# Kernel tuning notes

Hardware: AMD Instinct MI355X
Metric: run time of the kernel (lower is better)

Reference implementation:

```python
import jax, jax.numpy as jnp
import numpy as np
from jax import lax

MAX_CHARS = 50
EMB_DIM = 16
VOCAB = 263 + 1  # +1 padding row as in the torch module
FILTERS = [(1, 32), (2, 32), (3, 64), (4, 128), (5, 256), (6, 512), (7, 1024)]
TOTAL_FILTERS = sum(nf for _, nf in FILTERS)  # 2048
HIDDEN = 768
B, S = 8, 512


def setup_inputs() -> dict:
    key = jax.random.key(0)
    ks = list(jax.random.split(key, 32))
    pop = lambda: ks.pop()
    inp = {}
    inp["input_ids"] = jax.random.randint(pop(), (B, S, MAX_CHARS), 0, VOCAB, dtype=jnp.int32)
    inp["char_emb"] = jax.random.normal(pop(), (VOCAB, EMB_DIM), dtype=jnp.float32) * 0.02
    for i, (w, nf) in enumerate(FILTERS):
        inp[f"conv_w{i}"] = jax.random.normal(pop(), (nf, EMB_DIM, w), dtype=jnp.float32) * 0.05
        inp[f"conv_b{i}"] = jax.random.normal(pop(), (nf,), dtype=jnp.float32) * 0.02
    for j in range(2):  # highway layers, gate-bias half initialized to 1 as in torch code
        inp[f"hw_w{j}"] = jax.random.normal(pop(), (TOTAL_FILTERS, 2 * TOTAL_FILTERS), dtype=jnp.float32) * 0.02
        b_nl = jax.random.normal(pop(), (TOTAL_FILTERS,), dtype=jnp.float32) * 0.02
        inp[f"hw_b{j}"] = jnp.concatenate([b_nl, jnp.ones((TOTAL_FILTERS,), jnp.float32)])
    inp["proj_w"] = jax.random.normal(pop(), (TOTAL_FILTERS, HIDDEN), dtype=jnp.float32) * 0.02
    inp["proj_b"] = jax.random.normal(pop(), (HIDDEN,), dtype=jnp.float32) * 0.02
    return inp


def _char_cnn(input_ids, char_emb, conv_ws, conv_bs, hw_ws, hw_bs, proj_w, proj_b):
    token_dims = input_ids.shape[:-1]
    ids = input_ids.reshape(-1, MAX_CHARS)                     # [N, 50]
    x = char_emb[ids]                                          # [N, 50, 16]
    x = jnp.transpose(x, (0, 2, 1))                            # [N, C=16, L=50]
    outs = []
    for w_k, b_k in zip(conv_ws, conv_bs):
        y = lax.conv_general_dilated(x, w_k, window_strides=(1,), padding='VALID',
                                     dimension_numbers=('NCH', 'OIH', 'NCH'))
        y = y + b_k[None, :, None]                             # [N, nf, L-w+1]
        y = jax.nn.relu(jnp.max(y, axis=-1))                   # max-pool over positions, then relu
        outs.append(y)
    t = jnp.concatenate(outs, axis=-1)                         # [N, 2048]
    for hw_w, hw_b in zip(hw_ws, hw_bs):
        p = t @ hw_w + hw_b
        nl, gate = jnp.split(p, 2, axis=-1)
        g = jax.nn.sigmoid(gate)
        t = g * t + (1.0 - g) * jax.nn.relu(nl)
    out = t @ proj_w + proj_b                                  # [N, 768]
    return out.reshape(*token_dims, HIDDEN)


def reference(input_ids, char_emb,
              conv_w0, conv_b0, conv_w1, conv_b1, conv_w2, conv_b2, conv_w3, conv_b3,
              conv_w4, conv_b4, conv_w5, conv_b5, conv_w6, conv_b6,
              hw_w0, hw_b0, hw_w1, hw_b1, proj_w, proj_b):
    conv_ws = [conv_w0, conv_w1, conv_w2, conv_w3, conv_w4, conv_w5, conv_w6]
    conv_bs = [conv_b0, conv_b1, conv_b2, conv_b3, conv_b4, conv_b5, conv_b6]
    return _char_cnn(input_ids, char_emb, conv_ws, conv_bs,
                     [hw_w0, hw_w1], [hw_b0, hw_b1], proj_w, proj_b)
```

## Files before the change

kernel.cpp:

```cpp
#include <hip/hip_runtime.h>
#include <math.h>


#define NTOK 4096
#define NCHAR 50
#define EMB 16
#define TF 2048
#define HID 768
#define BK 64

typedef float f32x4 __attribute__((ext_vector_type(4)));
typedef _Float16 f16x8 __attribute__((ext_vector_type(8)));
typedef _Float16 half_t;

__device__ __forceinline__ void gl_lds16(const void* g, void* l) {
  __builtin_amdgcn_global_load_lds(
      (const __attribute__((address_space(1))) void*)g,
      (__attribute__((address_space(3))) void*)l, 16, 0, 0);
}

__global__ __launch_bounds__(256) void wpack_kernel(
    const float* __restrict__ w0, const float* __restrict__ w1,
    const float* __restrict__ w2, const float* __restrict__ w3,
    const float* __restrict__ w4, const float* __restrict__ w5,
    const float* __restrict__ w6,
    const float* __restrict__ b0, const float* __restrict__ b1,
    const float* __restrict__ b2, const float* __restrict__ b3,
    const float* __restrict__ b4, const float* __restrict__ b5,
    const float* __restrict__ b6,
    half_t* __restrict__ Wp, float* __restrict__ bias_all) {
  const int idx = blockIdx.x * 256 + threadIdx.x;
  if (idx < 219136) {
    int c, k, w; const float* src;
    if (idx < 1024)       { c = idx >> 5;             k = idx & 31;          w = 1; src = w0; }
    else if (idx < 2048)  { const int t = idx - 1024;  c = t >> 5; k = t & 31;  w = 2; src = w1; }
    else if (idx < 6144)  { const int t = idx - 2048;  c = t >> 6; k = t & 63;  w = 3; src = w2; }
    else if (idx < 14336) { const int t = idx - 6144;  c = t >> 6; k = t & 63;  w = 4; src = w3; }
    else if (idx < 38912) { const int t = idx - 14336; c = t / 96; k = t % 96;  w = 5; src = w4; }
    else if (idx < 88064) { const int t = idx - 38912; c = t / 96; k = t % 96;  w = 6; src = w5; }
    else                  { const int t = idx - 88064; c = t >> 7; k = t & 127; w = 7; src = w6; }
    const int j = k >> 4, i = k & 15;
    Wp[idx] = (half_t)((j < w) ? src[(c * EMB + i) * w + j] : 0.f);
  } else if (idx < 219136 + 2048) {
    const int c = idx - 219136;
    float v;
    if (c < 32)        v = b0[c];
    else if (c < 64)   v = b1[c - 32];
    else if (c < 128)  v = b2[c - 64];
    else if (c < 256)  v = b3[c - 128];
    else if (c < 512)  v = b4[c - 256];
    else if (c < 1024) v = b5[c - 512];
    else               v = b6[c - 1024];
    bias_all[c] = v;
  }
}


template<int MT, int KK, int NT, int L>
__device__ __forceinline__ void conv_mfma_worker(
    const char* myemb, float* pm,
    const half_t* __restrict__ Wp, const float* __restrict__ bias,
    half_t* __restrict__ outp, int kpad, int lane) {
  constexpr int S = NT * 16 + 8;
  const int l15 = lane & 15, l16 = lane >> 4;

  f16x8 a[MT][KK];
#pragma unroll
  for (int m = 0; m < MT; ++m)
#pragma unroll
    for (int kk = 0; kk < KK; ++kk) {
      const int row = m * 16 + l15 + 2 * kk + (l16 >> 1);
      a[m][kk] = *(const f16x8*)(myemb + row * 48 + (l16 & 1) * 16);
    }
#pragma unroll
  for (int m = 0; m < MT; ++m)
#pragma unroll
    for (int kk = 0; kk < KK; ++kk)
      asm volatile("" : "+v"(a[m][kk]));

  const half_t* bp = Wp + (size_t)l15 * kpad + l16 * 8;
  const size_t ntstep = (size_t)16 * kpad;

  auto group = [&](int nt, const f16x8 (&b)[KK]) {
    f32x4 acc[MT];
#pragma unroll
    for (int m = 0; m < MT; ++m) acc[m] = (f32x4){0.f, 0.f, 0.f, 0.f};
#pragma unroll
    for (int kk = 0; kk < KK; ++kk)
#pragma unroll
      for (int m = 0; m < MT; ++m)
        acc[m] = __builtin_amdgcn_mfma_f32_16x16x32_f16(a[m][kk], b[kk], acc[m], 0, 0, 0);
    float t[MT * 4];
#pragma unroll
    for (int m = 0; m < MT; ++m)
#pragma unroll
      for (int j = 0; j < 4; ++j) {
        const int pos = m * 16 + l16 * 4 + j;
        if ((m * 16 + 15) < L)
          t[m * 4 + j] = acc[m][j];
        else
          t[m * 4 + j] = (pos < L) ? acc[m][j] : -1e30f;
      }
#pragma unroll
    for (int s = 1; s < MT * 4; s *= 2)
#pragma unroll
      for (int i = 0; i + s < MT * 4; i += 2 * s)
        t[i] = fmaxf(t[i], t[i + s]);
    pm[l16 * S + nt * 16 + l15] = t[0];
  };

  f16x8 b0[KK], b1[KK];
#pragma unroll
  for (int kk = 0; kk < KK; ++kk) b0[kk] = *(const f16x8*)(bp + kk * 32);
#pragma unroll
  for (int nt = 0; nt < NT; nt += 2) {
#pragma unroll
    for (int kk = 0; kk < KK; ++kk)
      b1[kk] = *(const f16x8*)(bp + (size_t)(nt + 1) * ntstep + kk * 32);
    group(nt, b0);
    if (nt + 2 < NT) {
#pragma unroll
      for (int kk = 0; kk < KK; ++kk)
        b0[kk] = *(const f16x8*)(bp + (size_t)(nt + 2) * ntstep + kk * 32);
    }
    group(nt + 1, b1);
  }

#pragma unroll
  for (int c0 = 0; c0 < NT * 16; c0 += 64) {
    const int c = c0 + lane;
    if (c < NT * 16) {
      const float v0 = pm[0 * S + c], v1 = pm[1 * S + c];
      const float v2 = pm[2 * S + c], v3 = pm[3 * S + c];
      const float mx = fmaxf(fmaxf(v0, v1), fmaxf(v2, v3));
      outp[c] = (half_t)fmaxf(mx + bias[c], 0.f);
    }
  }
}

__global__ __launch_bounds__(256, 4) void conv_kernel(
    const int* __restrict__ ids, const float* __restrict__ cemb,
    const half_t* __restrict__ Wp, const float* __restrict__ bias_all,
    half_t* __restrict__ tout) {
  __shared__ char emb_s[4 * 72 * 48];
  __shared__ float pmax_s[4 * 4 * 264];
  const int tid = threadIdx.x, wave = tid >> 6, lane = tid & 63;
  const int tok = blockIdx.x * 4 + wave;
  char* myemb = emb_s + wave * (72 * 48);
  float* pm = pmax_s + wave * (4 * 264);

  for (int r = lane; r < 72; r += 64) {
    f16x8 lo, hi;
#pragma unroll
    for (int q = 0; q < 8; ++q) { lo[q] = (half_t)0.f; hi[q] = (half_t)0.f; }
    if (r < NCHAR) {
      const int id = ids[tok * NCHAR + r];
      const float4 v0 = *(const float4*)&cemb[id * EMB + 0];
      const float4 v1 = *(const float4*)&cemb[id * EMB + 4];
      const float4 v2 = *(const float4*)&cemb[id * EMB + 8];
      const float4 v3 = *(const float4*)&cemb[id * EMB + 12];
      lo[0] = (half_t)v0.x; lo[1] = (half_t)v0.y; lo[2] = (half_t)v0.z; lo[3] = (half_t)v0.w;
      lo[4] = (half_t)v1.x; lo[5] = (half_t)v1.y; lo[6] = (half_t)v1.z; lo[7] = (half_t)v1.w;
      hi[0] = (half_t)v2.x; hi[1] = (half_t)v2.y; hi[2] = (half_t)v2.z; hi[3] = (half_t)v2.w;
      hi[4] = (half_t)v3.x; hi[5] = (half_t)v3.y; hi[6] = (half_t)v3.z; hi[7] = (half_t)v3.w;
    }
    *(f16x8*)(myemb + r * 48) = lo;
    *(f16x8*)(myemb + r * 48 + 16) = hi;
  }

  half_t* outp = tout + (size_t)tok * TF;
  switch (blockIdx.y) {
    case 0:
      conv_mfma_worker<4, 1, 2, 50>(myemb, pm, Wp + 0,    bias_all + 0,   outp + 0,   32, lane);
      conv_mfma_worker<4, 1, 2, 49>(myemb, pm, Wp + 1024, bias_all + 32,  outp + 32,  32, lane);
      conv_mfma_worker<3, 2, 4, 48>(myemb, pm, Wp + 2048, bias_all + 64,  outp + 64,  64, lane);
      conv_mfma_worker<3, 2, 8, 47>(myemb, pm, Wp + 6144, bias_all + 128, outp + 128, 64, lane);
      break;
    case 1:  conv_mfma_worker<3, 3, 16, 46>(myemb, pm, Wp + 14336,  bias_all + 256,  outp + 256,  96,  lane); break;
    case 2:  conv_mfma_worker<3, 3, 16, 45>(myemb, pm, Wp + 38912,  bias_all + 512,  outp + 512,  96,  lane); break;
    case 3:  conv_mfma_worker<3, 3, 16, 45>(myemb, pm, Wp + 63488,  bias_all + 768,  outp + 768,  96,  lane); break;
    case 4:  conv_mfma_worker<3, 4, 16, 44>(myemb, pm, Wp + 88064,  bias_all + 1024, outp + 1024, 128, lane); break;
    case 5:  conv_mfma_worker<3, 4, 16, 44>(myemb, pm, Wp + 120832, bias_all + 1280, outp + 1280, 128, lane); break;
    case 6:  conv_mfma_worker<3, 4, 16, 44>(myemb, pm, Wp + 153600, bias_all + 1536, outp + 1536, 128, lane); break;
    default: conv_mfma_worker<3, 4, 16, 44>(myemb, pm, Wp + 186368, bias_all + 1792, outp + 1792, 128, lane); break;
  }
}

__global__ __launch_bounds__(256) void tcvt_kernel(
    const float* __restrict__ src, half_t* __restrict__ dst, int R, int C) {
  __shared__ half_t tile[64][72];
  const int tid = threadIdx.x;
  const int r0 = blockIdx.y * 64, c0 = blockIdx.x * 64;
  const int rr = tid >> 4, cq = tid & 15;
#pragma unroll
  for (int p = 0; p < 4; ++p) {
    const int r = rr + p * 16;
    const float4 v = *(const float4*)&src[(size_t)(r0 + r) * C + c0 + cq * 4];
    tile[cq * 4 + 0][r] = (half_t)v.x;
    tile[cq * 4 + 1][r] = (half_t)v.y;
    tile[cq * 4 + 2][r] = (half_t)v.z;
    tile[cq * 4 + 3][r] = (half_t)v.w;
  }
  __syncthreads();
#pragma unroll
  for (int p = 0; p < 2; ++p) {
    const int item = p * 256 + tid;
    const int c = item >> 3, ch = item & 7;
    const f16x8 v = *(const f16x8*)&tile[c][ch * 8];
    *(f16x8*)&dst[(size_t)(c0 + c) * R + r0 + ch * 8] = v;
  }
}

__global__ __launch_bounds__(256, 2) void highway_kernel(
    const half_t* __restrict__ tin, const half_t* __restrict__ Wt,
    const float* __restrict__ bv, half_t* __restrict__ tout) {
  __shared__ half_t smA[128 * BK];
  __shared__ half_t smBn[128 * BK];
  __shared__ half_t smBg[128 * BK];
  const int tid = threadIdx.x;
  const int wave = tid >> 6, lane = tid & 63;
  const int l15 = lane & 15, l16 = lane >> 4;
  const int wr = wave >> 1, wc = wave & 1;
  const int m0 = blockIdx.y * 128, n0 = blockIdx.x * 128;

  const char* Ab  = (const char*)tin + (size_t)m0 * (TF * 2);
  const char* Bnb = (const char*)Wt + (size_t)n0 * (TF * 2);
  const char* Bgb = (const char*)Wt + (size_t)(n0 + TF) * (TF * 2);

  f32x4 accn[4][4] = {};
  f32x4 accg[4][4] = {};

  for (int kt = 0; kt < TF / BK; ++kt) {
    if (kt) __syncthreads();
    const int kb0 = kt * (BK * 2);
#pragma unroll
    for (int i = 0; i < 4; ++i) {
      const int o = i * 4096 + tid * 16;
      const int row = o >> 7, kb = o & 127;
      const size_t gsrc = (size_t)row * (TF * 2) + kb0 + kb;
      gl_lds16(Ab + gsrc,  (char*)smA  + i * 4096 + wave * 1024);
      gl_lds16(Bnb + gsrc, (char*)smBn + i * 4096 + wave * 1024);
      gl_lds16(Bgb + gsrc, (char*)smBg + i * 4096 + wave * 1024);
    }
    __syncthreads();
#pragma unroll
    for (int ks = 0; ks < 2; ++ks) {
      f16x8 af[4], bn_[4], bg_[4];
#pragma unroll
      for (int m = 0; m < 4; ++m) {
        const int row = wr * 64 + m * 16 + l15;
        af[m] = *(const f16x8*)((const char*)smA + row * 128 + ks * 64 + l16 * 16);
      }
#pragma unroll
      for (int n = 0; n < 4; ++n) {
        const int row = wc * 64 + n * 16 + l15;
        bn_[n] = *(const f16x8*)((const char*)smBn + row * 128 + ks * 64 + l16 * 16);
        bg_[n] = *(const f16x8*)((const char*)smBg + row * 128 + ks * 64 + l16 * 16);
      }
#pragma unroll
      for (int m = 0; m < 4; ++m)
#pragma unroll
        for (int n = 0; n < 4; ++n) {
          accn[m][n] = __builtin_amdgcn_mfma_f32_16x16x32_f16(af[m], bn_[n], accn[m][n], 0, 0, 0);
          accg[m][n] = __builtin_amdgcn_mfma_f32_16x16x32_f16(af[m], bg_[n], accg[m][n], 0, 0, 0);
        }
    }
  }

#pragma unroll
  for (int n = 0; n < 4; ++n) {
    const int gn = n0 + wc * 64 + n * 16 + l15;
    const float bnl = bv[gn];
    const float bgt = bv[TF + gn];
#pragma unroll
    for (int m = 0; m < 4; ++m) {
#pragma unroll
      for (int j = 0; j < 4; ++j) {
        const int gm = m0 + wr * 64 + m * 16 + l16 * 4 + j;
        const float nl = accn[m][n][j] + bnl;
        const float gt = accg[m][n][j] + bgt;
        const float g = 1.f / (1.f + __expf(-gt));
        const float told = (float)tin[(size_t)gm * TF + gn];
        const float o = g * told + (1.f - g) * fmaxf(nl, 0.f);
        tout[(size_t)gm * TF + gn] = (half_t)o;
      }
    }
  }
}

__global__ __launch_bounds__(256, 2) void proj_kernel(
    const half_t* __restrict__ tin, const half_t* __restrict__ Wt,
    const float* __restrict__ bv, float* __restrict__ out) {
  __shared__ half_t smA[128 * BK];
  __shared__ half_t smB[128 * BK];
  const int tid = threadIdx.x;
  const int wave = tid >> 6, lane = tid & 63;
  const int l15 = lane & 15, l16 = lane >> 4;
  const int wr = wave >> 1, wc = wave & 1;
  const int m0 = blockIdx.y * 128, n0 = blockIdx.x * 128;

  const char* Ab = (const char*)tin + (size_t)m0 * (TF * 2);
  const char* Bb = (const char*)Wt + (size_t)n0 * (TF * 2);

  f32x4 acc[4][4] = {};

  for (int kt = 0; kt < TF / BK; ++kt) {
    if (kt) __syncthreads();
    const int kb0 = kt * (BK * 2);
#pragma unroll
    for (int i = 0; i < 4; ++i) {
      const int o = i * 4096 + tid * 16;
      const int row = o >> 7, kb = o & 127;
      const size_t gsrc = (size_t)row * (TF * 2) + kb0 + kb;
      gl_lds16(Ab + gsrc, (char*)smA + i * 4096 + wave * 1024);
      gl_lds16(Bb + gsrc, (char*)smB + i * 4096 + wave * 1024);
    }
    __syncthreads();
#pragma unroll
    for (int ks = 0; ks < 2; ++ks) {
      f16x8 af[4], bf[4];
#pragma unroll
      for (int m = 0; m < 4; ++m) {
        const int row = wr * 64 + m * 16 + l15;
        af[m] = *(const f16x8*)((const char*)smA + row * 128 + ks * 64 + l16 * 16);
      }
#pragma unroll
      for (int n = 0; n < 4; ++n) {
        const int row = wc * 64 + n * 16 + l15;
        bf[n] = *(const f16x8*)((const char*)smB + row * 128 + ks * 64 + l16 * 16);
      }
#pragma unroll
      for (int m = 0; m < 4; ++m)
#pragma unroll
        for (int n = 0; n < 4; ++n)
          acc[m][n] = __builtin_amdgcn_mfma_f32_16x16x32_f16(af[m], bf[n], acc[m][n], 0, 0, 0);
    }
  }

#pragma unroll
  for (int n = 0; n < 4; ++n) {
    const int gn = n0 + wc * 64 + n * 16 + l15;
    const float bb = bv[gn];
#pragma unroll
    for (int m = 0; m < 4; ++m) {
#pragma unroll
      for (int j = 0; j < 4; ++j) {
        const int gm = m0 + wr * 64 + m * 16 + l16 * 4 + j;
        out[(size_t)gm * HID + gn] = acc[m][n][j] + bb;
      }
    }
  }
}

extern "C" void kernel_launch(void* const* d_in, const int* in_sizes, int n_in,
                              void* d_out, int out_size, void* d_ws, size_t ws_size,
                              hipStream_t stream) {
  const int*   ids  = (const int*)d_in[0];
  const float* cemb = (const float*)d_in[1];
  const float* cw[7]; const float* cb[7];
  for (int i = 0; i < 7; ++i) {
    cw[i] = (const float*)d_in[2 + 2 * i];
    cb[i] = (const float*)d_in[3 + 2 * i];
  }
  const float* hw_w0  = (const float*)d_in[16];
  const float* hw_b0  = (const float*)d_in[17];
  const float* hw_w1  = (const float*)d_in[18];
  const float* hw_b1  = (const float*)d_in[19];
  const float* proj_w = (const float*)d_in[20];
  const float* proj_b = (const float*)d_in[21];
  float* out = (float*)d_out;

  char* ws = (char*)d_ws;
  half_t* t0h      = (half_t*)(ws);
  half_t* t1h      = (half_t*)(ws + 16777216);
  half_t* wbuf     = (half_t*)(ws + 33554432);
  float*  bias_all = (float*)(ws + 50331648);
  half_t* Wp       = (half_t*)(ws + 50339840);

  wpack_kernel<<<864, 256, 0, stream>>>(
      cw[0], cw[1], cw[2], cw[3], cw[4], cw[5], cw[6],
      cb[0], cb[1], cb[2], cb[3], cb[4], cb[5], cb[6], Wp, bias_all);

  conv_kernel<<<dim3(NTOK / 4, 8), 256, 0, stream>>>(ids, cemb, Wp, bias_all, t0h);

  tcvt_kernel<<<dim3(4096 / 64, TF / 64), 256, 0, stream>>>(hw_w0, wbuf, TF, 4096);
  highway_kernel<<<dim3(TF / 128, NTOK / 128), 256, 0, stream>>>(t0h, wbuf, hw_b0, t1h);

  tcvt_kernel<<<dim3(4096 / 64, TF / 64), 256, 0, stream>>>(hw_w1, wbuf, TF, 4096);
  highway_kernel<<<dim3(TF / 128, NTOK / 128), 256, 0, stream>>>(t1h, wbuf, hw_b1, t0h);

  tcvt_kernel<<<dim3(HID / 64, TF / 64), 256, 0, stream>>>(proj_w, wbuf, TF, HID);
  proj_kernel<<<dim3(HID / 128, NTOK / 128), 256, 0, stream>>>(t0h, wbuf, proj_b, out);
}
```

Measured before the change: 519.5 us.

## Pre-swizzle conv weights and GEMM LDS tiles into MFMA fragment order

Conv weights are packed so each lane's 16-byte B fragment for a given (nt, kk) sits contiguously, making the per-lane weight loads fully coalesced. The highway and projection GEMMs now fill LDS in 16x32 fragment blocks, so each wave reads its MFMA operands as linear 16-byte-per-lane chunks instead of row-strided 128-byte rows. The aim is to cut LDS bank conflicts and uncoalesced global reads. The packing index math grows, and the global loads feeding LDS become somewhat less contiguous per row.

```diff
diff --git a/kernel.cpp b/kernel.cpp
--- a/kernel.cpp
+++ b/kernel.cpp
@@ -19,7 +19,7 @@
       (__attribute__((address_space(3))) void*)l, 16, 0, 0);
 }
 
-__global__ __launch_bounds__(256) void wpack_kernel(
+__global__ __launch_bounds__(256) void wpack2_kernel(
     const float* __restrict__ w0, const float* __restrict__ w1,
     const float* __restrict__ w2, const float* __restrict__ w3,
     const float* __restrict__ w4, const float* __restrict__ w5,
@@ -28,19 +28,24 @@
     const float* __restrict__ b2, const float* __restrict__ b3,
     const float* __restrict__ b4, const float* __restrict__ b5,
     const float* __restrict__ b6,
-    half_t* __restrict__ Wp, float* __restrict__ bias_all) {
+    half_t* __restrict__ Wp2, float* __restrict__ bias_all) {
   const int idx = blockIdx.x * 256 + threadIdx.x;
   if (idx < 219136) {
-    int c, k, w; const float* src;
-    if (idx < 1024)       { c = idx >> 5;             k = idx & 31;          w = 1; src = w0; }
-    else if (idx < 2048)  { const int t = idx - 1024;  c = t >> 5; k = t & 31;  w = 2; src = w1; }
-    else if (idx < 6144)  { const int t = idx - 2048;  c = t >> 6; k = t & 63;  w = 3; src = w2; }
-    else if (idx < 14336) { const int t = idx - 6144;  c = t >> 6; k = t & 63;  w = 4; src = w3; }
-    else if (idx < 38912) { const int t = idx - 14336; c = t / 96; k = t % 96;  w = 5; src = w4; }
-    else if (idx < 88064) { const int t = idx - 38912; c = t / 96; k = t % 96;  w = 6; src = w5; }
-    else                  { const int t = idx - 88064; c = t >> 7; k = t & 127; w = 7; src = w6; }
+    int t, w, kpad; const float* src;
+    if (idx < 1024)       { t = idx;          w = 1; kpad = 32;  src = w0; }
+    else if (idx < 2048)  { t = idx - 1024;   w = 2; kpad = 32;  src = w1; }
+    else if (idx < 6144)  { t = idx - 2048;   w = 3; kpad = 64;  src = w2; }
+    else if (idx < 14336) { t = idx - 6144;   w = 4; kpad = 64;  src = w3; }
+    else if (idx < 38912) { t = idx - 14336;  w = 5; kpad = 96;  src = w4; }
+    else if (idx < 88064) { t = idx - 38912;  w = 6; kpad = 96;  src = w5; }
+    else                  { t = idx - 88064;  w = 7; kpad = 128; src = w6; }
+    const int e = t & 7, lane = (t >> 3) & 63, blk = t >> 9;
+    const int KKw = kpad >> 5;
+    const int kk = blk % KKw, nt = blk / KKw;
+    const int c = nt * 16 + (lane & 15);
+    const int k = kk * 32 + (lane >> 4) * 8 + e;
     const int j = k >> 4, i = k & 15;
-    Wp[idx] = (half_t)((j < w) ? src[(c * EMB + i) * w + j] : 0.f);
+    Wp2[idx] = (half_t)((j < w) ? src[(c * EMB + i) * w + j] : 0.f);
   } else if (idx < 219136 + 2048) {
     const int c = idx - 219136;
     float v;
@@ -57,10 +62,10 @@
 
 
 template<int MT, int KK, int NT, int L>
-__device__ __forceinline__ void conv_mfma_worker(
+__device__ __forceinline__ void conv_worker(
     const char* myemb, float* pm,
-    const half_t* __restrict__ Wp, const float* __restrict__ bias,
-    half_t* __restrict__ outp, int kpad, int lane) {
+    const half_t* __restrict__ W, const float* __restrict__ bias,
+    half_t* __restrict__ outp, int lane) {
   constexpr int S = NT * 16 + 8;
   const int l15 = lane & 15, l16 = lane >> 4;
 
@@ -78,8 +83,10 @@
     for (int kk = 0; kk < KK; ++kk)
       asm volatile("" : "+v"(a[m][kk]));
 
-  const half_t* bp = Wp + (size_t)l15 * kpad + l16 * 8;
-  const size_t ntstep = (size_t)16 * kpad;
+  const half_t* bpc = W + (size_t)lane * 8;
+  auto loadB = [&](int nt, int kk) -> f16x8 {
+    return *(const f16x8*)(bpc + (((size_t)nt * KK + kk) << 9));
+  };
 
   auto group = [&](int nt, const f16x8 (&b)[KK]) {
     f32x4 acc[MT];
@@ -111,17 +118,15 @@
 
   f16x8 b0[KK], b1[KK];
 #pragma unroll
-  for (int kk = 0; kk < KK; ++kk) b0[kk] = *(const f16x8*)(bp + kk * 32);
+  for (int kk = 0; kk < KK; ++kk) b0[kk] = loadB(0, kk);
 #pragma unroll
   for (int nt = 0; nt < NT; nt += 2) {
 #pragma unroll
-    for (int kk = 0; kk < KK; ++kk)
-      b1[kk] = *(const f16x8*)(bp + (size_t)(nt + 1) * ntstep + kk * 32);
+    for (int kk = 0; kk < KK; ++kk) b1[kk] = loadB(nt + 1, kk);
     group(nt, b0);
     if (nt + 2 < NT) {
 #pragma unroll
-      for (int kk = 0; kk < KK; ++kk)
-        b0[kk] = *(const f16x8*)(bp + (size_t)(nt + 2) * ntstep + kk * 32);
+      for (int kk = 0; kk < KK; ++kk) b0[kk] = loadB(nt + 2, kk);
     }
     group(nt + 1, b1);
   }
@@ -140,7 +145,7 @@
 
 __global__ __launch_bounds__(256, 4) void conv_kernel(
     const int* __restrict__ ids, const float* __restrict__ cemb,
-    const half_t* __restrict__ Wp, const float* __restrict__ bias_all,
+    const half_t* __restrict__ Wp2, const float* __restrict__ bias_all,
     half_t* __restrict__ tout) {
   __shared__ char emb_s[4 * 72 * 48];
   __shared__ float pmax_s[4 * 4 * 264];
@@ -171,18 +176,18 @@
   half_t* outp = tout + (size_t)tok * TF;
   switch (blockIdx.y) {
     case 0:
-      conv_mfma_worker<4, 1, 2, 50>(myemb, pm, Wp + 0,    bias_all + 0,   outp + 0,   32, lane);
-      conv_mfma_worker<4, 1, 2, 49>(myemb, pm, Wp + 1024, bias_all + 32,  outp + 32,  32, lane);
-      conv_mfma_worker<3, 2, 4, 48>(myemb, pm, Wp + 2048, bias_all + 64,  outp + 64,  64, lane);
-      conv_mfma_worker<3, 2, 8, 47>(myemb, pm, Wp + 6144, bias_all + 128, outp + 128, 64, lane);
+      conv_worker<4, 1, 2, 50>(myemb, pm, Wp2 + 0,    bias_all + 0,   outp + 0,   lane);
+      conv_worker<4, 1, 2, 49>(myemb, pm, Wp2 + 1024, bias_all + 32,  outp + 32,  lane);
+      conv_worker<3, 2, 4, 48>(myemb, pm, Wp2 + 2048, bias_all + 64,  outp + 64,  lane);
+      conv_worker<3, 2, 8, 47>(myemb, pm, Wp2 + 6144, bias_all + 128, outp + 128, lane);
       break;
-    case 1:  conv_mfma_worker<3, 3, 16, 46>(myemb, pm, Wp + 14336,  bias_all + 256,  outp + 256,  96,  lane); break;
-    case 2:  conv_mfma_worker<3, 3, 16, 45>(myemb, pm, Wp + 38912,  bias_all + 512,  outp + 512,  96,  lane); break;
-    case 3:  conv_mfma_worker<3, 3, 16, 45>(myemb, pm, Wp + 63488,  bias_all + 768,  outp + 768,  96,  lane); break;
-    case 4:  conv_mfma_worker<3, 4, 16, 44>(myemb, pm, Wp + 88064,  bias_all + 1024, outp + 1024, 128, lane); break;
-    case 5:  conv_mfma_worker<3, 4, 16, 44>(myemb, pm, Wp + 120832, bias_all + 1280, outp + 1280, 128, lane); break;
-    case 6:  conv_mfma_worker<3, 4, 16, 44>(myemb, pm, Wp + 153600, bias_all + 1536, outp + 1536, 128, lane); break;
-    default: conv_mfma_worker<3, 4, 16, 44>(myemb, pm, Wp + 186368, bias_all + 1792, outp + 1792, 128, lane); break;
+    case 1:  conv_worker<3, 3, 16, 46>(myemb, pm, Wp2 + 14336,  bias_all + 256,  outp + 256,  lane); break;
+    case 2:  conv_worker<3, 3, 16, 45>(myemb, pm, Wp2 + 38912,  bias_all + 512,  outp + 512,  lane); break;
+    case 3:  conv_worker<3, 3, 16, 45>(myemb, pm, Wp2 + 63488,  bias_all + 768,  outp + 768,  lane); break;
+    case 4:  conv_worker<3, 4, 16, 44>(myemb, pm, Wp2 + 88064,  bias_all + 1024, outp + 1024, lane); break;
+    case 5:  conv_worker<3, 4, 16, 44>(myemb, pm, Wp2 + 120832, bias_all + 1280, outp + 1280, lane); break;
+    case 6:  conv_worker<3, 4, 16, 44>(myemb, pm, Wp2 + 153600, bias_all + 1536, outp + 1536, lane); break;
+    default: conv_worker<3, 4, 16, 44>(myemb, pm, Wp2 + 186368, bias_all + 1792, outp + 1792, lane); break;
   }
 }
 
@@ -235,9 +240,10 @@
     const int kb0 = kt * (BK * 2);
 #pragma unroll
     for (int i = 0; i < 4; ++i) {
-      const int o = i * 4096 + tid * 16;
-      const int row = o >> 7, kb = o & 127;
-      const size_t gsrc = (size_t)row * (TF * 2) + kb0 + kb;
+      const int sub = i * 4 + wave;
+      const int row = (sub >> 1) * 16 + l15;
+      const int kcb = (sub & 1) * 64 + l16 * 16;
+      const size_t gsrc = (size_t)row * (TF * 2) + kb0 + kcb;
       gl_lds16(Ab + gsrc,  (char*)smA  + i * 4096 + wave * 1024);
       gl_lds16(Bnb + gsrc, (char*)smBn + i * 4096 + wave * 1024);
       gl_lds16(Bgb + gsrc, (char*)smBg + i * 4096 + wave * 1024);
@@ -247,15 +253,14 @@
     for (int ks = 0; ks < 2; ++ks) {
       f16x8 af[4], bn_[4], bg_[4];
 #pragma unroll
-      for (int m = 0; m < 4; ++m) {
-        const int row = wr * 64 + m * 16 + l15;
-        af[m] = *(const f16x8*)((const char*)smA + row * 128 + ks * 64 + l16 * 16);
-      }
+      for (int m = 0; m < 4; ++m)
+        af[m] = *(const f16x8*)((const char*)smA +
+                 ((((wr * 4 + m) * 2 + ks) * 64 + lane) << 4));
 #pragma unroll
       for (int n = 0; n < 4; ++n) {
-        const int row = wc * 64 + n * 16 + l15;
-        bn_[n] = *(const f16x8*)((const char*)smBn + row * 128 + ks * 64 + l16 * 16);
-        bg_[n] = *(const f16x8*)((const char*)smBg + row * 128 + ks * 64 + l16 * 16);
+        const int go = (((wc * 4 + n) * 2 + ks) * 64 + lane) << 4;
+        bn_[n] = *(const f16x8*)((const char*)smBn + go);
+        bg_[n] = *(const f16x8*)((const char*)smBg + go);
       }
 #pragma unroll
       for (int m = 0; m < 4; ++m)
@@ -309,9 +314,10 @@
     const int kb0 = kt * (BK * 2);
 #pragma unroll
     for (int i = 0; i < 4; ++i) {
-      const int o = i * 4096 + tid * 16;
-      const int row = o >> 7, kb = o & 127;
-      const size_t gsrc = (size_t)row * (TF * 2) + kb0 + kb;
+      const int sub = i * 4 + wave;
+      const int row = (sub >> 1) * 16 + l15;
+      const int kcb = (sub & 1) * 64 + l16 * 16;
+      const size_t gsrc = (size_t)row * (TF * 2) + kb0 + kcb;
       gl_lds16(Ab + gsrc, (char*)smA + i * 4096 + wave * 1024);
       gl_lds16(Bb + gsrc, (char*)smB + i * 4096 + wave * 1024);
     }
@@ -320,15 +326,13 @@
     for (int ks = 0; ks < 2; ++ks) {
       f16x8 af[4], bf[4];
 #pragma unroll
-      for (int m = 0; m < 4; ++m) {
-        const int row = wr * 64 + m * 16 + l15;
-        af[m] = *(const f16x8*)((const char*)smA + row * 128 + ks * 64 + l16 * 16);
-      }
-#pragma unroll
-      for (int n = 0; n < 4; ++n) {
-        const int row = wc * 64 + n * 16 + l15;
-        bf[n] = *(const f16x8*)((const char*)smB + row * 128 + ks * 64 + l16 * 16);
-      }
+      for (int m = 0; m < 4; ++m)
+        af[m] = *(const f16x8*)((const char*)smA +
+                 ((((wr * 4 + m) * 2 + ks) * 64 + lane) << 4));
+#pragma unroll
+      for (int n = 0; n < 4; ++n)
+        bf[n] = *(const f16x8*)((const char*)smB +
+                 ((((wc * 4 + n) * 2 + ks) * 64 + lane) << 4));
 #pragma unroll
       for (int m = 0; m < 4; ++m)
 #pragma unroll
@@ -375,13 +379,13 @@
   half_t* t1h      = (half_t*)(ws + 16777216);
   half_t* wbuf     = (half_t*)(ws + 33554432);
   float*  bias_all = (float*)(ws + 50331648);
-  half_t* Wp       = (half_t*)(ws + 50339840);
-
-  wpack_kernel<<<864, 256, 0, stream>>>(
+  half_t* Wp2      = (half_t*)(ws + 50339840);
+
+  wpack2_kernel<<<864, 256, 0, stream>>>(
       cw[0], cw[1], cw[2], cw[3], cw[4], cw[5], cw[6],
-      cb[0], cb[1], cb[2], cb[3], cb[4], cb[5], cb[6], Wp, bias_all);
-
-  conv_kernel<<<dim3(NTOK / 4, 8), 256, 0, stream>>>(ids, cemb, Wp, bias_all, t0h);
+      cb[0], cb[1], cb[2], cb[3], cb[4], cb[5], cb[6], Wp2, bias_all);
+
+  conv_kernel<<<dim3(NTOK / 4, 8), 256, 0, stream>>>(ids, cemb, Wp2, bias_all, t0h);
 
   tcvt_kernel<<<dim3(4096 / 64, TF / 64), 256, 0, stream>>>(hw_w0, wbuf, TF, 4096);
   highway_kernel<<<dim3(TF / 128, NTOK / 128), 256, 0, stream>>>(t0h, wbuf, hw_b0, t1h);
```

After: 473.5 us. 8.9% less time.
